# Optimization experiments

Hardware: AMD Instinct MI355X
Metric: run time of the kernel (lower is better)

The kernel has to match this reference:

```python
import jax, jax.numpy as jnp
import jax.scipy.linalg as jsl
import numpy as np

B, C_IN, T = 32, 64, 256
Z = 32
HID = [256, 256]
K = 3


def conv1d_same(x, W, b):
    # x: (B, C_in, T), W: (C_out, C_in, K) -> (B, C_out, T)
    y = jax.lax.conv_general_dilated(x, W, window_strides=(1,), padding='SAME',
                                     dimension_numbers=('NCH', 'OIH', 'NCH'))
    return y + b[None, :, None]


def setup_inputs() -> dict:
    key = jax.random.key(0)
    ks = jax.random.split(key, 4)
    scale = lambda fan_in: 1.0 / np.sqrt(fan_in)
    x = jax.random.normal(ks[0], (B, C_IN, T), dtype=jnp.float32)
    W0 = jax.random.normal(ks[1], (HID[0], C_IN, K), dtype=jnp.float32) * scale(C_IN * K)
    b0 = jnp.zeros((HID[0],), jnp.float32)
    W1 = jax.random.normal(ks[2], (HID[1], HID[0], K), dtype=jnp.float32) * scale(HID[0] * K)
    b1 = jnp.zeros((HID[1],), jnp.float32)
    W2 = jax.random.normal(ks[3], (3 * Z, HID[1], K), dtype=jnp.float32) * scale(HID[1] * K)
    b2 = jnp.zeros((3 * Z,), jnp.float32)
    return {"x": x, "W0": W0, "b0": b0, "W1": W1, "b1": b1, "W2": W2, "b2": b2}


def reference(x, W0, b0, W1, b1, W2, b2):
    batch, seq_len = x.shape[0], x.shape[-1]
    h = jax.nn.relu(conv1d_same(x, W0, b0))
    h = jax.nn.relu(conv1d_same(h, W1, b1))
    stats = conv1d_same(h, W2, b2)                       # (B, 3z, T)
    z = stats.shape[1] // 3
    mu = stats[:, :z]                                    # (B, z, T)
    prec = jax.nn.softplus(stats[:, z:])                 # (B, 2z, T), precision_activation
    # torch: reshape (B, 2z, T) -> (B, z, 2T), drop last value -> 2T-1 params per (b, z)
    prec = prec.reshape(batch, z, 2 * seq_len)[..., :-1]
    diag = prec[..., :seq_len]                           # (B, z, T)  diagonal entries
    sup = prec[..., seq_len:]                            # (B, z, T-1) superdiagonal entries
    # build upper-bidiagonal precision P = I + diag + superdiag
    i = jnp.arange(seq_len)
    j = jnp.arange(seq_len - 1)
    P = jnp.zeros((batch, z, seq_len, seq_len), dtype=x.dtype)
    P = P.at[..., i, i].set(diag + 1.0)
    P = P.at[..., j, j + 1].set(sup)
    eye = jnp.broadcast_to(jnp.eye(seq_len, dtype=x.dtype), P.shape)
    # covariance upper-triangular factor: solve P @ U = I (P upper triangular)
    cov_u = jsl.solve_triangular(P, eye, lower=False)
    cov_u = jnp.where(jnp.isfinite(cov_u), cov_u, jnp.zeros_like(cov_u))
    scale_tril = jnp.swapaxes(cov_u, -1, -2)             # lower triangular (B, z, T, T)
    return mu, scale_tril
```

## Files before the change

### kernel.cpp

```cpp
#include <hip/hip_runtime.h>
#include <hip/hip_bf16.h>
#include <math.h>

#define BB 32
#define TT 256
#define ZDIM 32

typedef float vf4 __attribute__((ext_vector_type(4)));
typedef short short8 __attribute__((ext_vector_type(8)));
typedef short short4v __attribute__((ext_vector_type(4)));
typedef float f32x4 __attribute__((ext_vector_type(4)));

__device__ __forceinline__ float softplus_f(float v) {
    return fmaxf(v, 0.0f) + log1pf(expf(-fabsf(v)));
}

__device__ __forceinline__ unsigned short f2bf(float f) {
    __hip_bfloat16 h = __float2bfloat16(f);
    return *reinterpret_cast<unsigned short*>(&h);
}

template<int COUT, int CIN>
__device__ void wconv_frag(const float* __restrict__ W, unsigned short* __restrict__ Wb,
                           int tid, int nthreads)
{
    const int n = 3 * COUT * CIN;
    for (int idx = tid; idx < n; idx += nthreads) {
        int j     = idx & 7;
        int lane  = (idx >> 3) & 63;
        int rest  = idx >> 9;
        int kch   = rest % (CIN / 32);
        int rest2 = rest / (CIN / 32);
        int ot    = rest2 % (COUT / 16);
        int ks    = rest2 / (COUT / 16);
        int o  = ot * 16 + (lane & 15);
        int ci = kch * 32 + (lane >> 4) * 8 + j;
        Wb[idx] = f2bf(W[(o * CIN + ci) * 3 + ks]);
    }
}

__global__ __launch_bounds__(256)
void wconv_kernel(const float* __restrict__ W0, const float* __restrict__ W1,
                  const float* __restrict__ W2, unsigned short* __restrict__ w0b,
                  unsigned short* __restrict__ w1b, unsigned short* __restrict__ w2b)
{
    const int tid = blockIdx.x * blockDim.x + threadIdx.x;
    const int nth = gridDim.x * blockDim.x;
    wconv_frag<256, 64>(W0, w0b, tid, nth);
    wconv_frag<256, 256>(W1, w1b, tid, nth);
    wconv_frag<96, 256>(W2, w2b, tid, nth);
}

__global__ __launch_bounds__(512, 1)
void fused_conv(const float* __restrict__ x,
                const unsigned short* __restrict__ w0b,
                const unsigned short* __restrict__ w1b,
                const unsigned short* __restrict__ w2b,
                const float* __restrict__ b0, const float* __restrict__ b1,
                const float* __restrict__ b2,
                float* __restrict__ mu, float* __restrict__ dd,
                float* __restrict__ ss)
{
    constexpr int XPAD = 72;
    constexpr int HPAD = 264;

    __shared__ __attribute__((aligned(16))) unsigned short xsb[64][XPAD];
    __shared__ __attribute__((aligned(16))) unsigned short h0s[48][HPAD];
    __shared__ __attribute__((aligned(16))) unsigned short h1s[34][HPAD];

    const int b    = blockIdx.x;
    const int t0   = blockIdx.y * 32;
    const int tid  = threadIdx.x;
    const int wv   = tid >> 6;
    const int lane = tid & 63;
    const int l15  = lane & 15;
    const int quad = lane >> 4;

    {
        const int ci = lane;
        const int t8 = t0 - 16 + wv * 8;
        unsigned short v[8];
        if (t8 >= 0 && t8 < TT) {
            const float* xp = x + (size_t)(b * 64 + ci) * TT + t8;
            f32x4 lo = *(const f32x4*)xp;
            f32x4 hi = *(const f32x4*)(xp + 4);
            #pragma unroll
            for (int j = 0; j < 4; ++j) { v[j] = f2bf(lo[j]); v[4 + j] = f2bf(hi[j]); }
        } else {
            #pragma unroll
            for (int j = 0; j < 8; ++j) v[j] = 0;
        }
        #pragma unroll
        for (int j = 0; j < 8; ++j) xsb[wv * 8 + j][ci] = v[j];
    }
    __syncthreads();

    {
        f32x4 a1[2][3];
        #pragma unroll
        for (int oi = 0; oi < 2; ++oi) {
            f32x4 bv;
            #pragma unroll
            for (int r = 0; r < 4; ++r) bv[r] = b0[(wv + 8 * oi) * 16 + quad * 4 + r];
            #pragma unroll
            for (int nt = 0; nt < 3; ++nt) a1[oi][nt] = bv;
        }
        #pragma unroll
        for (int ks = 0; ks < 3; ++ks) {
            #pragma unroll
            for (int kc = 0; kc < 64; kc += 32) {
                short8 af0 = *(const short8*)(w0b + (size_t)(((ks * 16 + wv) * 2) + (kc >> 5)) * 512 + lane * 8);
                short8 af1 = *(const short8*)(w0b + (size_t)(((ks * 16 + wv + 8) * 2) + (kc >> 5)) * 512 + lane * 8);
                #pragma unroll
                for (int nt = 0; nt < 3; ++nt) {
                    short8 bf = *(const short8*)&xsb[nt * 16 + l15 + ks + 7][kc + quad * 8];
                    a1[0][nt] = __builtin_amdgcn_mfma_f32_16x16x32_bf16(af0, bf, a1[0][nt], 0, 0, 0);
                    a1[1][nt] = __builtin_amdgcn_mfma_f32_16x16x32_bf16(af1, bf, a1[1][nt], 0, 0, 0);
                }
            }
        }
        #pragma unroll
        for (int oi = 0; oi < 2; ++oi) {
            #pragma unroll
            for (int nt = 0; nt < 3; ++nt) {
                int p = nt * 16 + l15;
                int t = t0 - 8 + p;
                bool ok = (t >= 0) && (t < TT);
                short4v v;
                #pragma unroll
                for (int r = 0; r < 4; ++r)
                    v[r] = ok ? (short)f2bf(fmaxf(a1[oi][nt][r], 0.f)) : (short)0;
                *(short4v*)&h0s[p][(wv + 8 * oi) * 16 + quad * 4] = v;
            }
        }
    }
    __syncthreads();

    {
        f32x4 a2[2][3];
        #pragma unroll
        for (int oi = 0; oi < 2; ++oi) {
            f32x4 bv;
            #pragma unroll
            for (int r = 0; r < 4; ++r) bv[r] = b1[(wv + 8 * oi) * 16 + quad * 4 + r];
            #pragma unroll
            for (int nt = 0; nt < 3; ++nt) a2[oi][nt] = bv;
        }
        #pragma unroll 1
        for (int c0 = 0; c0 < 256; c0 += 64) {
            #pragma unroll
            for (int ks = 0; ks < 3; ++ks) {
                #pragma unroll
                for (int kc = 0; kc < 64; kc += 32) {
                    short8 af0 = *(const short8*)(w1b + (size_t)((ks * 16 + wv) * 8 + ((c0 + kc) >> 5)) * 512 + lane * 8);
                    short8 af1 = *(const short8*)(w1b + (size_t)((ks * 16 + wv + 8) * 8 + ((c0 + kc) >> 5)) * 512 + lane * 8);
                    #pragma unroll
                    for (int nt = 0; nt < 3; ++nt) {
                        constexpr int F2[3] = {6, 22, 24};
                        short8 bf = *(const short8*)&h0s[F2[nt] + l15 + ks][c0 + kc + quad * 8];
                        a2[0][nt] = __builtin_amdgcn_mfma_f32_16x16x32_bf16(af0, bf, a2[0][nt], 0, 0, 0);
                        a2[1][nt] = __builtin_amdgcn_mfma_f32_16x16x32_bf16(af1, bf, a2[1][nt], 0, 0, 0);
                    }
                }
            }
        }
        #pragma unroll
        for (int oi = 0; oi < 2; ++oi) {
            #pragma unroll
            for (int nt = 0; nt < 3; ++nt) {
                constexpr int P2[3]  = {0, 16, 18};
                constexpr int TO2[3] = {-1, 15, 17};
                int p = P2[nt] + l15;
                int t = t0 + TO2[nt] + l15;
                bool ok = (t >= 0) && (t < TT);
                short4v v;
                #pragma unroll
                for (int r = 0; r < 4; ++r)
                    v[r] = ok ? (short)f2bf(fmaxf(a2[oi][nt][r], 0.f)) : (short)0;
                *(short4v*)&h1s[p][(wv + 8 * oi) * 16 + quad * 4] = v;
            }
        }
    }
    __syncthreads();

    {
        const int nu = (wv < 4) ? 2 : 1;
        for (int i = 0; i < nu; ++i) {
            const int u  = wv + 8 * i;
            const int ot = u % 6;
            const int nt = u / 6;
            f32x4 a3;
            #pragma unroll
            for (int r = 0; r < 4; ++r) a3[r] = b2[ot * 16 + quad * 4 + r];
            #pragma unroll 1
            for (int c0 = 0; c0 < 256; c0 += 64) {
                #pragma unroll
                for (int ks = 0; ks < 3; ++ks) {
                    #pragma unroll
                    for (int kc = 0; kc < 64; kc += 32) {
                        short8 af = *(const short8*)(w2b + (size_t)((ks * 6 + ot) * 8 + ((c0 + kc) >> 5)) * 512 + lane * 8);
                        short8 bf = *(const short8*)&h1s[nt * 16 + l15 + ks][c0 + kc + quad * 8];
                        a3 = __builtin_amdgcn_mfma_f32_16x16x32_bf16(af, bf, a3, 0, 0, 0);
                    }
                }
            }
            const int t = t0 + nt * 16 + l15;
            #pragma unroll
            for (int r = 0; r < 4; ++r) {
                int o = ot * 16 + quad * 4 + r;
                float val = a3[r];
                if (o < ZDIM) {
                    mu[(b * ZDIM + o) * TT + t] = val;
                } else {
                    int oc = o - ZDIM;
                    int z  = oc >> 1;
                    float sp = softplus_f(val);
                    if ((oc & 1) == 0) dd[(b * ZDIM + z) * TT + t] = sp + 1.f;
                    else               ss[(b * ZDIM + z) * TT + t] = sp;
                }
            }
        }
    }
}

__global__ __launch_bounds__(256)
void tril_kernel(const float* __restrict__ dd, const float* __restrict__ ss,
                 float* __restrict__ out)
{
    __shared__ float invd[TT];
    __shared__ float tt[TT];

    const int bz  = blockIdx.x;
    const int tid = threadIdx.x;

    {
        float d  = dd[bz * TT + tid];
        float s  = ss[bz * TT + tid];
        float iv = 1.0f / d;
        invd[tid] = iv;
        tt[tid]   = -s * iv;
    }
    __syncthreads();

    const int r0 = (tid >> 6) * 64;
    const int c0 = (tid & 63) * 4;

    float p0 = 1.f, p1 = 1.f, p2 = 1.f, p3 = 1.f;
    for (int k = 0; k < r0 - 1; ++k) {
        float tm = tt[k];
        p0 = (k >= c0    ) ? p0 * tm : p0;
        p1 = (k >= c0 + 1) ? p1 * tm : p1;
        p2 = (k >= c0 + 2) ? p2 * tm : p2;
        p3 = (k >= c0 + 3) ? p3 * tm : p3;
    }
    p0 = (c0     < r0) ? p0 : 0.f;
    p1 = (c0 + 1 < r0) ? p1 : 0.f;
    p2 = (c0 + 2 < r0) ? p2 : 0.f;
    p3 = (c0 + 3 < r0) ? p3 : 0.f;

    float* orow = out + (size_t)bz * TT * TT + (size_t)r0 * TT + c0;

    #pragma unroll 2
    for (int r = r0; r < r0 + 64; ++r) {
        float tm = (r > 0) ? tt[r - 1] : 0.0f;
        p0 = (r == c0    ) ? 1.0f : p0 * tm;
        p1 = (r == c0 + 1) ? 1.0f : p1 * tm;
        p2 = (r == c0 + 2) ? 1.0f : p2 * tm;
        p3 = (r == c0 + 3) ? 1.0f : p3 * tm;
        float id = invd[r];
        vf4 v;
        v.x = p0 * id; v.y = p1 * id; v.z = p2 * id; v.w = p3 * id;
        v.x = isfinite(v.x) ? v.x : 0.0f;
        v.y = isfinite(v.y) ? v.y : 0.0f;
        v.z = isfinite(v.z) ? v.z : 0.0f;
        v.w = isfinite(v.w) ? v.w : 0.0f;
        __builtin_nontemporal_store(v, (vf4*)orow);
        orow += TT;
    }
}

extern "C" void kernel_launch(void* const* d_in, const int* in_sizes, int n_in,
                              void* d_out, int out_size, void* d_ws, size_t ws_size,
                              hipStream_t stream)
{
    const float* x  = (const float*)d_in[0];
    const float* W0 = (const float*)d_in[1];
    const float* b0 = (const float*)d_in[2];
    const float* W1 = (const float*)d_in[3];
    const float* b1 = (const float*)d_in[4];
    const float* W2 = (const float*)d_in[5];
    const float* b2 = (const float*)d_in[6];

    float* out = (float*)d_out;
    float* mu  = out;
    float* st  = out + BB * ZDIM * TT;

    float* dd = (float*)d_ws;
    float* ss = dd + BB * ZDIM * TT;
    unsigned short* w0b = (unsigned short*)(ss + BB * ZDIM * TT);
    unsigned short* w1b = w0b + 3 * 256 * 64;
    unsigned short* w2b = w1b + 3 * 256 * 256;

    wconv_kernel<<<dim3(256), 256, 0, stream>>>(W0, W1, W2, w0b, w1b, w2b);
    fused_conv<<<dim3(BB, 8), 512, 0, stream>>>(
        x, w0b, w1b, w2b, b0, b1, b2, mu, dd, ss);
    tril_kernel<<<dim3(BB * ZDIM), 256, 0, stream>>>(dd, ss, st);
}
```

Measured before the change: 303.4 us.

## Double fused_conv block to 1024 threads, one output tile per wave

The fused conv kernel now launches 16 waves per block instead of 8. Each wave computes a single 16-channel output tile in layers 0 and 1, and the final layer spreads its 12 tiles across 12 waves instead of looping. This raises parallelism within the 256-block grid, which is smaller than the CU count, at the cost of more redundant LDS reads of activations and lower per-wave register reuse of the B fragments.

```diff
diff --git a/kernel.cpp b/kernel.cpp
--- a/kernel.cpp
+++ b/kernel.cpp
@@ -51,7 +51,7 @@
     wconv_frag<96, 256>(W2, w2b, tid, nth);
 }
 
-__global__ __launch_bounds__(512, 1)
+__global__ __launch_bounds__(1024, 1)
 void fused_conv(const float* __restrict__ x,
                 const unsigned short* __restrict__ w0b,
                 const unsigned short* __restrict__ w1b,
@@ -76,7 +76,7 @@
     const int l15  = lane & 15;
     const int quad = lane >> 4;
 
-    {
+    if (wv < 8) {
         const int ci = lane;
         const int t8 = t0 - 16 + wv * 8;
         unsigned short v[8];
@@ -96,55 +96,48 @@
     __syncthreads();
 
     {
-        f32x4 a1[2][3];
-        #pragma unroll
-        for (int oi = 0; oi < 2; ++oi) {
+        f32x4 a1[3];
+        {
             f32x4 bv;
             #pragma unroll
-            for (int r = 0; r < 4; ++r) bv[r] = b0[(wv + 8 * oi) * 16 + quad * 4 + r];
-            #pragma unroll
-            for (int nt = 0; nt < 3; ++nt) a1[oi][nt] = bv;
+            for (int r = 0; r < 4; ++r) bv[r] = b0[wv * 16 + quad * 4 + r];
+            #pragma unroll
+            for (int nt = 0; nt < 3; ++nt) a1[nt] = bv;
         }
         #pragma unroll
         for (int ks = 0; ks < 3; ++ks) {
             #pragma unroll
             for (int kc = 0; kc < 64; kc += 32) {
-                short8 af0 = *(const short8*)(w0b + (size_t)(((ks * 16 + wv) * 2) + (kc >> 5)) * 512 + lane * 8);
-                short8 af1 = *(const short8*)(w0b + (size_t)(((ks * 16 + wv + 8) * 2) + (kc >> 5)) * 512 + lane * 8);
+                short8 af = *(const short8*)(w0b + (size_t)((ks * 16 + wv) * 2 + (kc >> 5)) * 512 + lane * 8);
                 #pragma unroll
                 for (int nt = 0; nt < 3; ++nt) {
                     short8 bf = *(const short8*)&xsb[nt * 16 + l15 + ks + 7][kc + quad * 8];
-                    a1[0][nt] = __builtin_amdgcn_mfma_f32_16x16x32_bf16(af0, bf, a1[0][nt], 0, 0, 0);
-                    a1[1][nt] = __builtin_amdgcn_mfma_f32_16x16x32_bf16(af1, bf, a1[1][nt], 0, 0, 0);
+                    a1[nt] = __builtin_amdgcn_mfma_f32_16x16x32_bf16(af, bf, a1[nt], 0, 0, 0);
                 }
             }
         }
         #pragma unroll
-        for (int oi = 0; oi < 2; ++oi) {
-            #pragma unroll
-            for (int nt = 0; nt < 3; ++nt) {
-                int p = nt * 16 + l15;
-                int t = t0 - 8 + p;
-                bool ok = (t >= 0) && (t < TT);
-                short4v v;
-                #pragma unroll
-                for (int r = 0; r < 4; ++r)
-                    v[r] = ok ? (short)f2bf(fmaxf(a1[oi][nt][r], 0.f)) : (short)0;
-                *(short4v*)&h0s[p][(wv + 8 * oi) * 16 + quad * 4] = v;
-            }
+        for (int nt = 0; nt < 3; ++nt) {
+            int p = nt * 16 + l15;
+            int t = t0 - 8 + p;
+            bool ok = (t >= 0) && (t < TT);
+            short4v v;
+            #pragma unroll
+            for (int r = 0; r < 4; ++r)
+                v[r] = ok ? (short)f2bf(fmaxf(a1[nt][r], 0.f)) : (short)0;
+            *(short4v*)&h0s[p][wv * 16 + quad * 4] = v;
         }
     }
     __syncthreads();
 
     {
-        f32x4 a2[2][3];
-        #pragma unroll
-        for (int oi = 0; oi < 2; ++oi) {
+        f32x4 a2[3];
+        {
             f32x4 bv;
             #pragma unroll
-            for (int r = 0; r < 4; ++r) bv[r] = b1[(wv + 8 * oi) * 16 + quad * 4 + r];
-            #pragma unroll
-            for (int nt = 0; nt < 3; ++nt) a2[oi][nt] = bv;
+            for (int r = 0; r < 4; ++r) bv[r] = b1[wv * 16 + quad * 4 + r];
+            #pragma unroll
+            for (int nt = 0; nt < 3; ++nt) a2[nt] = bv;
         }
         #pragma unroll 1
         for (int c0 = 0; c0 < 256; c0 += 64) {
@@ -152,72 +145,63 @@
             for (int ks = 0; ks < 3; ++ks) {
                 #pragma unroll
                 for (int kc = 0; kc < 64; kc += 32) {
-                    short8 af0 = *(const short8*)(w1b + (size_t)((ks * 16 + wv) * 8 + ((c0 + kc) >> 5)) * 512 + lane * 8);
-                    short8 af1 = *(const short8*)(w1b + (size_t)((ks * 16 + wv + 8) * 8 + ((c0 + kc) >> 5)) * 512 + lane * 8);
+                    short8 af = *(const short8*)(w1b + (size_t)((ks * 16 + wv) * 8 + ((c0 + kc) >> 5)) * 512 + lane * 8);
                     #pragma unroll
                     for (int nt = 0; nt < 3; ++nt) {
                         constexpr int F2[3] = {6, 22, 24};
                         short8 bf = *(const short8*)&h0s[F2[nt] + l15 + ks][c0 + kc + quad * 8];
-                        a2[0][nt] = __builtin_amdgcn_mfma_f32_16x16x32_bf16(af0, bf, a2[0][nt], 0, 0, 0);
-                        a2[1][nt] = __builtin_amdgcn_mfma_f32_16x16x32_bf16(af1, bf, a2[1][nt], 0, 0, 0);
+                        a2[nt] = __builtin_amdgcn_mfma_f32_16x16x32_bf16(af, bf, a2[nt], 0, 0, 0);
                     }
                 }
             }
         }
         #pragma unroll
-        for (int oi = 0; oi < 2; ++oi) {
-            #pragma unroll
-            for (int nt = 0; nt < 3; ++nt) {
-                constexpr int P2[3]  = {0, 16, 18};
-                constexpr int TO2[3] = {-1, 15, 17};
-                int p = P2[nt] + l15;
-                int t = t0 + TO2[nt] + l15;
-                bool ok = (t >= 0) && (t < TT);
-                short4v v;
+        for (int nt = 0; nt < 3; ++nt) {
+            constexpr int P2[3]  = {0, 16, 18};
+            constexpr int TO2[3] = {-1, 15, 17};
+            int p = P2[nt] + l15;
+            int t = t0 + TO2[nt] + l15;
+            bool ok = (t >= 0) && (t < TT);
+            short4v v;
+            #pragma unroll
+            for (int r = 0; r < 4; ++r)
+                v[r] = ok ? (short)f2bf(fmaxf(a2[nt][r], 0.f)) : (short)0;
+            *(short4v*)&h1s[p][wv * 16 + quad * 4] = v;
+        }
+    }
+    __syncthreads();
+
+    if (wv < 12) {
+        const int ot = wv % 6;
+        const int nt = wv / 6;
+        f32x4 a3;
+        #pragma unroll
+        for (int r = 0; r < 4; ++r) a3[r] = b2[ot * 16 + quad * 4 + r];
+        #pragma unroll 1
+        for (int c0 = 0; c0 < 256; c0 += 64) {
+            #pragma unroll
+            for (int ks = 0; ks < 3; ++ks) {
                 #pragma unroll
-                for (int r = 0; r < 4; ++r)
-                    v[r] = ok ? (short)f2bf(fmaxf(a2[oi][nt][r], 0.f)) : (short)0;
-                *(short4v*)&h1s[p][(wv + 8 * oi) * 16 + quad * 4] = v;
-            }
-        }
-    }
-    __syncthreads();
-
-    {
-        const int nu = (wv < 4) ? 2 : 1;
-        for (int i = 0; i < nu; ++i) {
-            const int u  = wv + 8 * i;
-            const int ot = u % 6;
-            const int nt = u / 6;
-            f32x4 a3;
-            #pragma unroll
-            for (int r = 0; r < 4; ++r) a3[r] = b2[ot * 16 + quad * 4 + r];
-            #pragma unroll 1
-            for (int c0 = 0; c0 < 256; c0 += 64) {
-                #pragma unroll
-                for (int ks = 0; ks < 3; ++ks) {
-                    #pragma unroll
-                    for (int kc = 0; kc < 64; kc += 32) {
-                        short8 af = *(const short8*)(w2b + (size_t)((ks * 6 + ot) * 8 + ((c0 + kc) >> 5)) * 512 + lane * 8);
-                        short8 bf = *(const short8*)&h1s[nt * 16 + l15 + ks][c0 + kc + quad * 8];
-                        a3 = __builtin_amdgcn_mfma_f32_16x16x32_bf16(af, bf, a3, 0, 0, 0);
-                    }
+                for (int kc = 0; kc < 64; kc += 32) {
+                    short8 af = *(const short8*)(w2b + (size_t)((ks * 6 + ot) * 8 + ((c0 + kc) >> 5)) * 512 + lane * 8);
+                    short8 bf = *(const short8*)&h1s[nt * 16 + l15 + ks][c0 + kc + quad * 8];
+                    a3 = __builtin_amdgcn_mfma_f32_16x16x32_bf16(af, bf, a3, 0, 0, 0);
                 }
             }
-            const int t = t0 + nt * 16 + l15;
-            #pragma unroll
-            for (int r = 0; r < 4; ++r) {
-                int o = ot * 16 + quad * 4 + r;
-                float val = a3[r];
-                if (o < ZDIM) {
-                    mu[(b * ZDIM + o) * TT + t] = val;
-                } else {
-                    int oc = o - ZDIM;
-                    int z  = oc >> 1;
-                    float sp = softplus_f(val);
-                    if ((oc & 1) == 0) dd[(b * ZDIM + z) * TT + t] = sp + 1.f;
-                    else               ss[(b * ZDIM + z) * TT + t] = sp;
-                }
+        }
+        const int t = t0 + nt * 16 + l15;
+        #pragma unroll
+        for (int r = 0; r < 4; ++r) {
+            int o = ot * 16 + quad * 4 + r;
+            float val = a3[r];
+            if (o < ZDIM) {
+                mu[(b * ZDIM + o) * TT + t] = val;
+            } else {
+                int oc = o - ZDIM;
+                int z  = oc >> 1;
+                float sp = softplus_f(val);
+                if ((oc & 1) == 0) dd[(b * ZDIM + z) * TT + t] = sp + 1.f;
+                else               ss[(b * ZDIM + z) * TT + t] = sp;
             }
         }
     }
@@ -302,7 +286,7 @@
     unsigned short* w2b = w1b + 3 * 256 * 256;
 
     wconv_kernel<<<dim3(256), 256, 0, stream>>>(W0, W1, W2, w0b, w1b, w2b);
-    fused_conv<<<dim3(BB, 8), 512, 0, stream>>>(
+    fused_conv<<<dim3(BB, 8), 1024, 0, stream>>>(
         x, w0b, w1b, w2b, b0, b1, b2, mu, dd, ss);
     tril_kernel<<<dim3(BB * ZDIM), 256, 0, stream>>>(dd, ss, st);
 }
```

After: 300.0 us. About the same (-1.1%).
